# Performance work log

Measured on AMD Instinct MI355X. Metric: run time of the kernel, lower is better.

The kernel has to match this reference:

```python
import jax, jax.numpy as jnp
import numpy as np

TEMPERATURE = 0.1

def setup_inputs() -> dict:
    key = jax.random.key(0)
    k1, k2 = jax.random.split(key)
    B, D = 8192, 512
    anchor = jax.random.normal(k1, (B, D), dtype=jnp.float32)
    positive = jax.random.normal(k2, (B, D), dtype=jnp.float32)
    return {"anchor": anchor, "positive": positive}

def reference(anchor, positive):
    # sim[i, j] = <anchor_i, positive_j> / T  -- [B, B]
    sim = jnp.einsum("bd,nd->bn", anchor, positive) / TEMPERATURE
    # InfoNCE with in-batch negatives: positive is the diagonal; since softmax
    # is permutation-invariant, -log_softmax(logits)[pos] = logsumexp(row) - diag.
    loss = jax.nn.logsumexp(sim, axis=1) - jnp.diagonal(sim)
    return jnp.mean(loss)
```

## Files before the change

kernel.cpp:

```cpp
#include <hip/hip_runtime.h>
#include <hip/hip_bf16.h>
#include <math.h>
#include <stdint.h>


#define NB 8192
#define DDIM 512
#define SPLITS 16
#define BM 256
#define BN 128
#define CPB (NB / SPLITS)
#define TPB (CPB / BN)
#define NROUND 32

#define DELTA 0.045f
#define INV_DELTA (1.0f / DELTA)
#define OUT_SCALE (DELTA * DELTA * 10.0f)

typedef unsigned char u8;
typedef __attribute__((ext_vector_type(4))) int i32x4;

__device__ __forceinline__ void gl2lds16(const u8* g, const u8* l) {
  __builtin_amdgcn_global_load_lds(
      (__attribute__((address_space(1))) unsigned int*)(uintptr_t)g,
      (__attribute__((address_space(3))) unsigned int*)(unsigned int)(uintptr_t)l,
      16, 0, 0);
}

__device__ __forceinline__ unsigned pack4(float x0, float x1, float x2, float x3) {
  int q0 = min(127, max(-127, __float2int_rn(x0 * INV_DELTA)));
  int q1 = min(127, max(-127, __float2int_rn(x1 * INV_DELTA)));
  int q2 = min(127, max(-127, __float2int_rn(x2 * INV_DELTA)));
  int q3 = min(127, max(-127, __float2int_rn(x3 * INV_DELTA)));
  return (q0 & 0xFF) | ((q1 & 0xFF) << 8) | ((q2 & 0xFF) << 16) | ((q3 & 0xFF) << 24);
}

__global__ void cvt_diag_kernel(const float* __restrict__ a, const float* __restrict__ p,
                                u8* __restrict__ aq, u8* __restrict__ pq,
                                float* __restrict__ diag, float* __restrict__ out) {
  if (blockIdx.x == 0 && threadIdx.x == 0) out[0] = 0.f;
  int row = (blockIdx.x * 256 + threadIdx.x) >> 6;
  int lane = threadIdx.x & 63;
  const float4* ar = (const float4*)(a + (size_t)row * DDIM + lane * 8);
  const float4* pr = (const float4*)(p + (size_t)row * DDIM + lane * 8);
  float4 a0 = ar[0], a1 = ar[1];
  float4 p0 = pr[0], p1 = pr[1];
  *(uint2*)(aq + (size_t)row * DDIM + lane * 8) =
      (uint2){pack4(a0.x, a0.y, a0.z, a0.w), pack4(a1.x, a1.y, a1.z, a1.w)};
  *(uint2*)(pq + (size_t)row * DDIM + lane * 8) =
      (uint2){pack4(p0.x, p0.y, p0.z, p0.w), pack4(p1.x, p1.y, p1.z, p1.w)};
  float s = a0.x * p0.x + a0.y * p0.y + a0.z * p0.z + a0.w * p0.w +
            a1.x * p1.x + a1.y * p1.y + a1.z * p1.z + a1.w * p1.w;
  for (int off = 32; off > 0; off >>= 1) s += __shfl_down(s, off);
  if (lane == 0) diag[row] = s * 10.0f;
}

__global__ __launch_bounds__(512, 4) void gemm_lse(
    const u8* __restrict__ Aq, const u8* __restrict__ Bq,
    float* __restrict__ partM, float* __restrict__ partL) {
  __shared__ u8 sA[2][BM * 64];
  __shared__ u8 sB[2][BN * 64];
  __shared__ float sMm[2][BM];
  __shared__ float sMl[2][BM];

  const int tid = threadIdx.x;
  const int wave = tid >> 6;
  const int lane = tid & 63;
  const int quad = lane >> 4;
  const int l16 = lane & 15;
  const int wr = wave >> 1, wc = wave & 1;

  const int bid = blockIdx.x;
  const int xcd = bid & 7;
  const int idx = bid >> 3;
  const int rowTile = (idx & 3) * 8 + xcd;
  const int colSplit = idx >> 2;
  const int row0 = rowTile * BM;
  const int col0 = colSplit * CPB;

  const int rsub = lane >> 2;
  const int qsrc = (lane & 3) ^ ((rsub >> 1) & 3);
  const u8* aCol = Aq + (size_t)(row0 + wave * 32 + rsub) * DDIM + qsrc * 16;
  const u8* bCol = Bq + (size_t)(col0 + wave * 16 + rsub) * DDIM + qsrc * 16;
  const int ldsOffA = wave * 2048;
  const int ldsOffB = wave * 1024;

  const int sw = (l16 >> 1) & 3;
  const int fragA = (wr * 64 + l16) * 64 + ((quad ^ sw) * 16);
  const int fragB = (wc * 64 + l16) * 64 + ((quad ^ sw) * 16);

#define STAGE(r)                                                        \
  do {                                                                  \
    int _t = (r) >> 3, _kk = ((r) & 7) << 6, _bf = (r) & 1;             \
    const u8* _a = aCol + _kk;                                          \
    const u8* _b = bCol + _t * (BN * DDIM) + _kk;                       \
    gl2lds16(_a, &sA[_bf][ldsOffA]);                                    \
    gl2lds16(_a + 16 * DDIM, &sA[_bf][ldsOffA + 1024]);                 \
    gl2lds16(_b, &sB[_bf][ldsOffB]);                                    \
  } while (0)

  STAGE(0);

  i32x4 acc[4][4];
#pragma unroll
  for (int mi = 0; mi < 4; ++mi)
#pragma unroll
    for (int ni = 0; ni < 4; ++ni) acc[mi][ni] = (i32x4){0, 0, 0, 0};

  float rm[4][4], rl[4][4];
#pragma unroll
  for (int mi = 0; mi < 4; ++mi)
#pragma unroll
    for (int rr = 0; rr < 4; ++rr) { rm[mi][rr] = -INFINITY; rl[mi][rr] = 0.f; }

  for (int r = 0; r < NROUND; ++r) {
    const int buf = r & 1;
    __syncthreads();
    if (r < NROUND - 1) STAGE(r + 1);

    i32x4 bq[4];
#pragma unroll
    for (int ni = 0; ni < 4; ++ni)
      bq[ni] = *(const i32x4*)(&sB[buf][fragB + ni * 16 * 64]);
#pragma unroll
    for (int mi = 0; mi < 4; ++mi) {
      i32x4 af = *(const i32x4*)(&sA[buf][fragA + mi * 16 * 64]);
#pragma unroll
      for (int ni = 0; ni < 4; ++ni)
        acc[mi][ni] = __builtin_amdgcn_mfma_i32_16x16x64_i8(af, bq[ni], acc[mi][ni], 0, 0, 0);
    }

    if ((r & 7) == 7) {
#pragma unroll
      for (int mi = 0; mi < 4; ++mi) {
#pragma unroll
        for (int rr = 0; rr < 4; ++rr) {
          float v0 = (float)acc[mi][0][rr] * OUT_SCALE;
          float v1 = (float)acc[mi][1][rr] * OUT_SCALE;
          float v2 = (float)acc[mi][2][rr] * OUT_SCALE;
          float v3 = (float)acc[mi][3][rr] * OUT_SCALE;
          float vm = fmaxf(fmaxf(v0, v1), fmaxf(v2, v3));
          float nm = fmaxf(rm[mi][rr], vm);
          rl[mi][rr] = rl[mi][rr] * __expf(rm[mi][rr] - nm) +
                       (__expf(v0 - nm) + __expf(v1 - nm) +
                        __expf(v2 - nm) + __expf(v3 - nm));
          rm[mi][rr] = nm;
#pragma unroll
          for (int ni = 0; ni < 4; ++ni) acc[mi][ni][rr] = 0;
        }
      }
    }
  }

#pragma unroll
  for (int mi = 0; mi < 4; ++mi) {
#pragma unroll
    for (int rr = 0; rr < 4; ++rr) {
      float m = rm[mi][rr], l = rl[mi][rr];
#pragma unroll
      for (int mask = 1; mask < 16; mask <<= 1) {
        float om = __shfl_xor(m, mask);
        float ol = __shfl_xor(l, mask);
        float nm = fmaxf(m, om);
        l = l * __expf(m - nm) + ol * __expf(om - nm);
        m = nm;
      }
      if (l16 == 0) {
        int rowl = wr * 64 + mi * 16 + quad * 4 + rr;
        sMm[wc][rowl] = m;
        sMl[wc][rowl] = l;
      }
    }
  }
  __syncthreads();
  if (tid < BM) {
    float m0 = sMm[0][tid], m1 = sMm[1][tid];
    float l0 = sMl[0][tid], l1 = sMl[1][tid];
    float nm = fmaxf(m0, m1);
    partM[(size_t)colSplit * NB + row0 + tid] = nm;
    partL[(size_t)colSplit * NB + row0 + tid] =
        l0 * __expf(m0 - nm) + l1 * __expf(m1 - nm);
  }
#undef STAGE
}

__global__ void reduce_kernel(const float* __restrict__ partM,
                              const float* __restrict__ partL,
                              const float* __restrict__ diag, float* __restrict__ out) {
  __shared__ float red[4];
  int r = blockIdx.x * 256 + threadIdx.x;
  float M = -INFINITY;
#pragma unroll
  for (int s = 0; s < SPLITS; ++s) M = fmaxf(M, partM[(size_t)s * NB + r]);
  float L = 0.f;
#pragma unroll
  for (int s = 0; s < SPLITS; ++s)
    L += partL[(size_t)s * NB + r] * __expf(partM[(size_t)s * NB + r] - M);
  float v = M + __logf(L) - diag[r];
  for (int off = 32; off > 0; off >>= 1) v += __shfl_down(v, off);
  if ((threadIdx.x & 63) == 0) red[threadIdx.x >> 6] = v;
  __syncthreads();
  if (threadIdx.x == 0) {
    float s = (red[0] + red[1] + red[2] + red[3]) * (1.0f / (float)NB);
    atomicAdd(out, s);
  }
}

extern "C" void kernel_launch(void* const* d_in, const int* in_sizes, int n_in,
                              void* d_out, int out_size, void* d_ws, size_t ws_size,
                              hipStream_t stream) {
  const float* anchor = (const float*)d_in[0];
  const float* positive = (const float*)d_in[1];
  float* out = (float*)d_out;

  char* ws = (char*)d_ws;
  u8* Aq = (u8*)ws;
  u8* Bq = (u8*)(ws + (size_t)4194304);
  float* diag = (float*)(ws + (size_t)8388608);
  float* partM = (float*)(ws + (size_t)8388608 + 32768);
  float* partL = (float*)(ws + (size_t)8388608 + 32768 + (size_t)SPLITS * NB * 4);

  cvt_diag_kernel<<<NB / 4, 256, 0, stream>>>(anchor, positive, Aq, Bq, diag, out);
  gemm_lse<<<512, 512, 0, stream>>>(Aq, Bq, partM, partL);
  reduce_kernel<<<NB / 256, 256, 0, stream>>>(partM, partL, diag, out);
}
```

Measured before the change: 126.6 us.

## Use 256x256 tiles with single K pass and base-2 LSE partials

Each block now computes a square 256x256 tile over the full K dimension, with each wave holding an 8x4 set of MFMA accumulators. There are 32 column splits instead of 16 splits that each looped over four 128-column tiles, so the grid becomes 1024 blocks. The LSE epilogue runs once at the end, uses integer max and exp2/log2, reuses LDS as scratch, and stores a single log-sum-exp partial per row instead of separate max and sum. This raises arithmetic intensity per LDS load and cuts epilogue and partial-store traffic. In exchange it doubles accumulator registers, lowers occupancy (launch bounds 2) and shortens each block's pipeline to 8 steps.

```diff
diff --git a/kernel.cpp b/kernel.cpp
--- a/kernel.cpp
+++ b/kernel.cpp
@@ -6,19 +6,34 @@
 
 #define NB 8192
 #define DDIM 512
-#define SPLITS 16
+#define SPLITS 32
 #define BM 256
-#define BN 128
-#define CPB (NB / SPLITS)
-#define TPB (CPB / BN)
-#define NROUND 32
+#define BNB 256
+#define KT 8
 
 #define DELTA 0.045f
 #define INV_DELTA (1.0f / DELTA)
 #define OUT_SCALE (DELTA * DELTA * 10.0f)
+#define K2F (OUT_SCALE * 1.4426950408889634f)
+#define LN2F 0.6931471805599453f
 
 typedef unsigned char u8;
 typedef __attribute__((ext_vector_type(4))) int i32x4;
+
+__device__ __forceinline__ float fexp2(float x) {
+#if __has_builtin(__builtin_amdgcn_exp2f)
+  return __builtin_amdgcn_exp2f(x);
+#else
+  return __expf(x * LN2F);
+#endif
+}
+__device__ __forceinline__ float flog2(float x) {
+#if __has_builtin(__builtin_amdgcn_logf)
+  return __builtin_amdgcn_logf(x);
+#else
+  return __logf(x) * 1.4426950408889634f;
+#endif
+}
 
 __device__ __forceinline__ void gl2lds16(const u8* g, const u8* l) {
   __builtin_amdgcn_global_load_lds(
@@ -55,20 +70,19 @@
   if (lane == 0) diag[row] = s * 10.0f;
 }
 
-__global__ __launch_bounds__(512, 4) void gemm_lse(
+__global__ __launch_bounds__(512, 2) void gemm_lse(
     const u8* __restrict__ Aq, const u8* __restrict__ Bq,
-    float* __restrict__ partM, float* __restrict__ partL) {
+    float* __restrict__ partLse) {
   __shared__ u8 sA[2][BM * 64];
-  __shared__ u8 sB[2][BN * 64];
-  __shared__ float sMm[2][BM];
-  __shared__ float sMl[2][BM];
+  __shared__ u8 sB[2][BNB * 64];
 
   const int tid = threadIdx.x;
   const int wave = tid >> 6;
   const int lane = tid & 63;
   const int quad = lane >> 4;
   const int l16 = lane & 15;
-  const int wr = wave >> 1, wc = wave & 1;
+  const int wr = wave >> 2;
+  const int wc = wave & 3;
 
   const int bid = blockIdx.x;
   const int xcd = bid & 7;
@@ -76,127 +90,119 @@
   const int rowTile = (idx & 3) * 8 + xcd;
   const int colSplit = idx >> 2;
   const int row0 = rowTile * BM;
-  const int col0 = colSplit * CPB;
+  const int col0 = colSplit * BNB;
 
   const int rsub = lane >> 2;
   const int qsrc = (lane & 3) ^ ((rsub >> 1) & 3);
   const u8* aCol = Aq + (size_t)(row0 + wave * 32 + rsub) * DDIM + qsrc * 16;
-  const u8* bCol = Bq + (size_t)(col0 + wave * 16 + rsub) * DDIM + qsrc * 16;
-  const int ldsOffA = wave * 2048;
-  const int ldsOffB = wave * 1024;
+  const u8* bCol = Bq + (size_t)(col0 + wave * 32 + rsub) * DDIM + qsrc * 16;
+  const int ldsOff = wave * 2048;
 
   const int sw = (l16 >> 1) & 3;
-  const int fragA = (wr * 64 + l16) * 64 + ((quad ^ sw) * 16);
+  const int fragA = (wr * 128 + l16) * 64 + ((quad ^ sw) * 16);
   const int fragB = (wc * 64 + l16) * 64 + ((quad ^ sw) * 16);
 
-#define STAGE(r)                                                        \
-  do {                                                                  \
-    int _t = (r) >> 3, _kk = ((r) & 7) << 6, _bf = (r) & 1;             \
-    const u8* _a = aCol + _kk;                                          \
-    const u8* _b = bCol + _t * (BN * DDIM) + _kk;                       \
-    gl2lds16(_a, &sA[_bf][ldsOffA]);                                    \
-    gl2lds16(_a + 16 * DDIM, &sA[_bf][ldsOffA + 1024]);                 \
-    gl2lds16(_b, &sB[_bf][ldsOffB]);                                    \
-  } while (0)
-
-  STAGE(0);
-
-  i32x4 acc[4][4];
-#pragma unroll
-  for (int mi = 0; mi < 4; ++mi)
+  gl2lds16(aCol, &sA[0][ldsOff]);
+  gl2lds16(aCol + 16 * DDIM, &sA[0][ldsOff + 1024]);
+  gl2lds16(bCol, &sB[0][ldsOff]);
+  gl2lds16(bCol + 16 * DDIM, &sB[0][ldsOff + 1024]);
+
+  i32x4 acc[8][4];
+#pragma unroll
+  for (int mi = 0; mi < 8; ++mi)
 #pragma unroll
     for (int ni = 0; ni < 4; ++ni) acc[mi][ni] = (i32x4){0, 0, 0, 0};
 
-  float rm[4][4], rl[4][4];
-#pragma unroll
-  for (int mi = 0; mi < 4; ++mi)
-#pragma unroll
-    for (int rr = 0; rr < 4; ++rr) { rm[mi][rr] = -INFINITY; rl[mi][rr] = 0.f; }
-
-  for (int r = 0; r < NROUND; ++r) {
-    const int buf = r & 1;
+  float2* const scr0 = (float2*)&sA[0][0];
+  float2* const scr1 = (float2*)&sB[0][0];
+
+  for (int kt = 0; kt < KT; ++kt) {
+    const int par = kt & 1;
     __syncthreads();
-    if (r < NROUND - 1) STAGE(r + 1);
-
+    if (kt < KT - 1) {
+      const int kk = (kt + 1) * 64;
+      gl2lds16(aCol + kk, &sA[par ^ 1][ldsOff]);
+      gl2lds16(aCol + 16 * DDIM + kk, &sA[par ^ 1][ldsOff + 1024]);
+      gl2lds16(bCol + kk, &sB[par ^ 1][ldsOff]);
+      gl2lds16(bCol + 16 * DDIM + kk, &sB[par ^ 1][ldsOff + 1024]);
+    }
     i32x4 bq[4];
 #pragma unroll
     for (int ni = 0; ni < 4; ++ni)
-      bq[ni] = *(const i32x4*)(&sB[buf][fragB + ni * 16 * 64]);
-#pragma unroll
-    for (int mi = 0; mi < 4; ++mi) {
-      i32x4 af = *(const i32x4*)(&sA[buf][fragA + mi * 16 * 64]);
+      bq[ni] = *(const i32x4*)(&sB[par][fragB + ni * 1024]);
+#pragma unroll
+    for (int mp = 0; mp < 4; ++mp) {
+      i32x4 a0 = *(const i32x4*)(&sA[par][fragA + (2 * mp) * 1024]);
+      i32x4 a1 = *(const i32x4*)(&sA[par][fragA + (2 * mp + 1) * 1024]);
 #pragma unroll
       for (int ni = 0; ni < 4; ++ni)
-        acc[mi][ni] = __builtin_amdgcn_mfma_i32_16x16x64_i8(af, bq[ni], acc[mi][ni], 0, 0, 0);
-    }
-
-    if ((r & 7) == 7) {
-#pragma unroll
-      for (int mi = 0; mi < 4; ++mi) {
-#pragma unroll
-        for (int rr = 0; rr < 4; ++rr) {
-          float v0 = (float)acc[mi][0][rr] * OUT_SCALE;
-          float v1 = (float)acc[mi][1][rr] * OUT_SCALE;
-          float v2 = (float)acc[mi][2][rr] * OUT_SCALE;
-          float v3 = (float)acc[mi][3][rr] * OUT_SCALE;
-          float vm = fmaxf(fmaxf(v0, v1), fmaxf(v2, v3));
-          float nm = fmaxf(rm[mi][rr], vm);
-          rl[mi][rr] = rl[mi][rr] * __expf(rm[mi][rr] - nm) +
-                       (__expf(v0 - nm) + __expf(v1 - nm) +
-                        __expf(v2 - nm) + __expf(v3 - nm));
-          rm[mi][rr] = nm;
-#pragma unroll
-          for (int ni = 0; ni < 4; ++ni) acc[mi][ni][rr] = 0;
+        acc[2 * mp][ni] =
+            __builtin_amdgcn_mfma_i32_16x16x64_i8(a0, bq[ni], acc[2 * mp][ni], 0, 0, 0);
+#pragma unroll
+      for (int ni = 0; ni < 4; ++ni)
+        acc[2 * mp + 1][ni] =
+            __builtin_amdgcn_mfma_i32_16x16x64_i8(a1, bq[ni], acc[2 * mp + 1][ni], 0, 0, 0);
+      if (kt == KT - 1) {
+#pragma unroll
+        for (int mi = 2 * mp; mi <= 2 * mp + 1; ++mi) {
+#pragma unroll
+          for (int rr = 0; rr < 4; ++rr) {
+            const int i0 = acc[mi][0][rr], i1 = acc[mi][1][rr];
+            const int i2 = acc[mi][2][rr], i3 = acc[mi][3][rr];
+            const int im = max(max(i0, i1), max(i2, i3));
+            const float mf = (float)im * K2F;
+            float l = fexp2(fmaf((float)i0, K2F, -mf)) +
+                      fexp2(fmaf((float)i1, K2F, -mf)) +
+                      fexp2(fmaf((float)i2, K2F, -mf)) +
+                      fexp2(fmaf((float)i3, K2F, -mf));
+            float m = mf;
+#pragma unroll
+            for (int mask = 1; mask < 4; mask <<= 1) {
+              const float om = __shfl_xor(m, mask);
+              const float ol = __shfl_xor(l, mask);
+              const float nm = fmaxf(m, om);
+              l = l * fexp2(m - nm) + ol * fexp2(om - nm);
+              m = nm;
+            }
+            if ((l16 & 3) == 0) {
+              const int rowl = mi * 16 + quad * 4 + rr;
+              (wr ? scr1 : scr0)[rowl * 16 + (l16 >> 2) * 4 + wc] = (float2){m, l};
+            }
+          }
         }
       }
     }
   }
 
-#pragma unroll
-  for (int mi = 0; mi < 4; ++mi) {
-#pragma unroll
-    for (int rr = 0; rr < 4; ++rr) {
-      float m = rm[mi][rr], l = rl[mi][rr];
-#pragma unroll
-      for (int mask = 1; mask < 16; mask <<= 1) {
-        float om = __shfl_xor(m, mask);
-        float ol = __shfl_xor(l, mask);
-        float nm = fmaxf(m, om);
-        l = l * __expf(m - nm) + ol * __expf(om - nm);
-        m = nm;
-      }
-      if (l16 == 0) {
-        int rowl = wr * 64 + mi * 16 + quad * 4 + rr;
-        sMm[wc][rowl] = m;
-        sMl[wc][rowl] = l;
-      }
-    }
-  }
   __syncthreads();
   if (tid < BM) {
-    float m0 = sMm[0][tid], m1 = sMm[1][tid];
-    float l0 = sMl[0][tid], l1 = sMl[1][tid];
-    float nm = fmaxf(m0, m1);
-    partM[(size_t)colSplit * NB + row0 + tid] = nm;
-    partL[(size_t)colSplit * NB + row0 + tid] =
-        l0 * __expf(m0 - nm) + l1 * __expf(m1 - nm);
+    const float2* scr = (tid < 128) ? scr0 : scr1;
+    const int rowl = tid & 127;
+    float2 p[16];
+    float M = -INFINITY;
+#pragma unroll
+    for (int i = 0; i < 16; ++i) {
+      p[i] = scr[rowl * 16 + i];
+      M = fmaxf(M, p[i].x);
+    }
+    float L = 0.f;
+#pragma unroll
+    for (int i = 0; i < 16; ++i) L += p[i].y * fexp2(p[i].x - M);
+    partLse[(size_t)colSplit * NB + row0 + tid] = M + flog2(L);
   }
-#undef STAGE
-}
-
-__global__ void reduce_kernel(const float* __restrict__ partM,
-                              const float* __restrict__ partL,
+}
+
+__global__ void reduce_kernel(const float* __restrict__ partLse,
                               const float* __restrict__ diag, float* __restrict__ out) {
   __shared__ float red[4];
   int r = blockIdx.x * 256 + threadIdx.x;
   float M = -INFINITY;
 #pragma unroll
-  for (int s = 0; s < SPLITS; ++s) M = fmaxf(M, partM[(size_t)s * NB + r]);
+  for (int s = 0; s < SPLITS; ++s) M = fmaxf(M, partLse[(size_t)s * NB + r]);
   float L = 0.f;
 #pragma unroll
-  for (int s = 0; s < SPLITS; ++s)
-    L += partL[(size_t)s * NB + r] * __expf(partM[(size_t)s * NB + r] - M);
-  float v = M + __logf(L) - diag[r];
+  for (int s = 0; s < SPLITS; ++s) L += fexp2(partLse[(size_t)s * NB + r] - M);
+  float v = (M + flog2(L)) * LN2F - diag[r];
   for (int off = 32; off > 0; off >>= 1) v += __shfl_down(v, off);
   if ((threadIdx.x & 63) == 0) red[threadIdx.x >> 6] = v;
   __syncthreads();
@@ -217,10 +223,9 @@
   u8* Aq = (u8*)ws;
   u8* Bq = (u8*)(ws + (size_t)4194304);
   float* diag = (float*)(ws + (size_t)8388608);
-  float* partM = (float*)(ws + (size_t)8388608 + 32768);
-  float* partL = (float*)(ws + (size_t)8388608 + 32768 + (size_t)SPLITS * NB * 4);
+  float* partLse = (float*)(ws + (size_t)8388608 + 32768);
 
   cvt_diag_kernel<<<NB / 4, 256, 0, stream>>>(anchor, positive, Aq, Bq, diag, out);
-  gemm_lse<<<512, 512, 0, stream>>>(Aq, Bq, partM, partL);
-  reduce_kernel<<<NB / 256, 256, 0, stream>>>(partM, partL, diag, out);
-}
+  gemm_lse<<<SPLITS * (NB / BM), 512, 0, stream>>>(Aq, Bq, partLse);
+  reduce_kernel<<<NB / 256, 256, 0, stream>>>(partLse, diag, out);
+}
```

Result: slower. 133.1 us (+5.1%).

## Switch to 32x32x32 int8 MFMA with base-2 online LSE and single partial buffer

Applied to the files above, without the earlier changes.

Replaces the 16x16x64 int8 MFMA tiling with 32x32x32 MFMAs, so each wave issues fewer, larger matrix ops and uses a different fragment layout and row mapping. The online logsumexp moves to base-2 exponentials with the scale folded into a single FMA, and the per-row max is taken in the integer domain before conversion. Each split now writes one log-sum-exp value instead of separate max and sum arrays, which cuts partial-buffer traffic in the reduce. The larger MFMA reduces LDS fragment reads per MAC but changes the register layout and needs a wider 32-lane shuffle reduction.

```diff
diff --git a/kernel.cpp b/kernel.cpp
--- a/kernel.cpp
+++ b/kernel.cpp
@@ -10,15 +10,32 @@
 #define BM 256
 #define BN 128
 #define CPB (NB / SPLITS)
-#define TPB (CPB / BN)
 #define NROUND 32
 
 #define DELTA 0.045f
 #define INV_DELTA (1.0f / DELTA)
 #define OUT_SCALE (DELTA * DELTA * 10.0f)
+#define K2F (OUT_SCALE * 1.4426950408889634f)
+#define LN2F 0.6931471805599453f
 
 typedef unsigned char u8;
 typedef __attribute__((ext_vector_type(4))) int i32x4;
+typedef __attribute__((ext_vector_type(16))) int i32x16;
+
+__device__ __forceinline__ float fexp2(float x) {
+#if __has_builtin(__builtin_amdgcn_exp2f)
+  return __builtin_amdgcn_exp2f(x);
+#else
+  return __expf(x * LN2F);
+#endif
+}
+__device__ __forceinline__ float flog2(float x) {
+#if __has_builtin(__builtin_amdgcn_logf)
+  return __builtin_amdgcn_logf(x);
+#else
+  return __logf(x) * 1.4426950408889634f;
+#endif
+}
 
 __device__ __forceinline__ void gl2lds16(const u8* g, const u8* l) {
   __builtin_amdgcn_global_load_lds(
@@ -57,7 +74,7 @@
 
 __global__ __launch_bounds__(512, 4) void gemm_lse(
     const u8* __restrict__ Aq, const u8* __restrict__ Bq,
-    float* __restrict__ partM, float* __restrict__ partL) {
+    float* __restrict__ partLse) {
   __shared__ u8 sA[2][BM * 64];
   __shared__ u8 sB[2][BN * 64];
   __shared__ float sMm[2][BM];
@@ -66,8 +83,8 @@
   const int tid = threadIdx.x;
   const int wave = tid >> 6;
   const int lane = tid & 63;
-  const int quad = lane >> 4;
-  const int l16 = lane & 15;
+  const int l32 = lane & 31;
+  const int hi = lane >> 5;
   const int wr = wave >> 1, wc = wave & 1;
 
   const int bid = blockIdx.x;
@@ -85,9 +102,11 @@
   const int ldsOffA = wave * 2048;
   const int ldsOffB = wave * 1024;
 
-  const int sw = (l16 >> 1) & 3;
-  const int fragA = (wr * 64 + l16) * 64 + ((quad ^ sw) * 16);
-  const int fragB = (wc * 64 + l16) * 64 + ((quad ^ sw) * 16);
+  const int sw32 = (l32 >> 1) & 3;
+  const int oct0 = ((0 + hi) ^ sw32) * 16;
+  const int oct1 = ((2 + hi) ^ sw32) * 16;
+  const int rowA = (wr * 64 + l32) * 64;
+  const int rowB = (wc * 64 + l32) * 64;
 
 #define STAGE(r)                                                        \
   do {                                                                  \
@@ -101,72 +120,78 @@
 
   STAGE(0);
 
-  i32x4 acc[4][4];
-#pragma unroll
-  for (int mi = 0; mi < 4; ++mi)
-#pragma unroll
-    for (int ni = 0; ni < 4; ++ni) acc[mi][ni] = (i32x4){0, 0, 0, 0};
-
-  float rm[4][4], rl[4][4];
-#pragma unroll
-  for (int mi = 0; mi < 4; ++mi)
-#pragma unroll
-    for (int rr = 0; rr < 4; ++rr) { rm[mi][rr] = -INFINITY; rl[mi][rr] = 0.f; }
+  i32x16 acc[2][2];
+#pragma unroll
+  for (int mb = 0; mb < 2; ++mb)
+#pragma unroll
+    for (int nb = 0; nb < 2; ++nb)
+#pragma unroll
+      for (int g = 0; g < 16; ++g) acc[mb][nb][g] = 0;
+
+  float rm[2][16], rl[2][16];
+#pragma unroll
+  for (int mb = 0; mb < 2; ++mb)
+#pragma unroll
+    for (int g = 0; g < 16; ++g) { rm[mb][g] = -INFINITY; rl[mb][g] = 0.f; }
 
   for (int r = 0; r < NROUND; ++r) {
     const int buf = r & 1;
     __syncthreads();
     if (r < NROUND - 1) STAGE(r + 1);
 
-    i32x4 bq[4];
-#pragma unroll
-    for (int ni = 0; ni < 4; ++ni)
-      bq[ni] = *(const i32x4*)(&sB[buf][fragB + ni * 16 * 64]);
-#pragma unroll
-    for (int mi = 0; mi < 4; ++mi) {
-      i32x4 af = *(const i32x4*)(&sA[buf][fragA + mi * 16 * 64]);
-#pragma unroll
-      for (int ni = 0; ni < 4; ++ni)
-        acc[mi][ni] = __builtin_amdgcn_mfma_i32_16x16x64_i8(af, bq[ni], acc[mi][ni], 0, 0, 0);
-    }
+    i32x4 b0k0 = *(const i32x4*)(&sB[buf][rowB + 0 * 2048 + oct0]);
+    i32x4 b1k0 = *(const i32x4*)(&sB[buf][rowB + 1 * 2048 + oct0]);
+    i32x4 b0k1 = *(const i32x4*)(&sB[buf][rowB + 0 * 2048 + oct1]);
+    i32x4 b1k1 = *(const i32x4*)(&sB[buf][rowB + 1 * 2048 + oct1]);
+    i32x4 a0k0 = *(const i32x4*)(&sA[buf][rowA + 0 * 2048 + oct0]);
+    i32x4 a1k0 = *(const i32x4*)(&sA[buf][rowA + 1 * 2048 + oct0]);
+    i32x4 a0k1 = *(const i32x4*)(&sA[buf][rowA + 0 * 2048 + oct1]);
+    i32x4 a1k1 = *(const i32x4*)(&sA[buf][rowA + 1 * 2048 + oct1]);
+
+    acc[0][0] = __builtin_amdgcn_mfma_i32_32x32x32_i8(a0k0, b0k0, acc[0][0], 0, 0, 0);
+    acc[0][1] = __builtin_amdgcn_mfma_i32_32x32x32_i8(a0k0, b1k0, acc[0][1], 0, 0, 0);
+    acc[1][0] = __builtin_amdgcn_mfma_i32_32x32x32_i8(a1k0, b0k0, acc[1][0], 0, 0, 0);
+    acc[1][1] = __builtin_amdgcn_mfma_i32_32x32x32_i8(a1k0, b1k0, acc[1][1], 0, 0, 0);
+    acc[0][0] = __builtin_amdgcn_mfma_i32_32x32x32_i8(a0k1, b0k1, acc[0][0], 0, 0, 0);
+    acc[0][1] = __builtin_amdgcn_mfma_i32_32x32x32_i8(a0k1, b1k1, acc[0][1], 0, 0, 0);
+    acc[1][0] = __builtin_amdgcn_mfma_i32_32x32x32_i8(a1k1, b0k1, acc[1][0], 0, 0, 0);
+    acc[1][1] = __builtin_amdgcn_mfma_i32_32x32x32_i8(a1k1, b1k1, acc[1][1], 0, 0, 0);
 
     if ((r & 7) == 7) {
 #pragma unroll
-      for (int mi = 0; mi < 4; ++mi) {
-#pragma unroll
-        for (int rr = 0; rr < 4; ++rr) {
-          float v0 = (float)acc[mi][0][rr] * OUT_SCALE;
-          float v1 = (float)acc[mi][1][rr] * OUT_SCALE;
-          float v2 = (float)acc[mi][2][rr] * OUT_SCALE;
-          float v3 = (float)acc[mi][3][rr] * OUT_SCALE;
-          float vm = fmaxf(fmaxf(v0, v1), fmaxf(v2, v3));
-          float nm = fmaxf(rm[mi][rr], vm);
-          rl[mi][rr] = rl[mi][rr] * __expf(rm[mi][rr] - nm) +
-                       (__expf(v0 - nm) + __expf(v1 - nm) +
-                        __expf(v2 - nm) + __expf(v3 - nm));
-          rm[mi][rr] = nm;
-#pragma unroll
-          for (int ni = 0; ni < 4; ++ni) acc[mi][ni][rr] = 0;
+      for (int mb = 0; mb < 2; ++mb) {
+#pragma unroll
+        for (int g = 0; g < 16; ++g) {
+          const int i0 = acc[mb][0][g], i1 = acc[mb][1][g];
+          const int im = max(i0, i1);
+          const float mf = (float)im * K2F;
+          const float nm = fmaxf(rm[mb][g], mf);
+          rl[mb][g] = rl[mb][g] * fexp2(rm[mb][g] - nm) +
+                      fexp2(fmaf((float)i0, K2F, -nm)) +
+                      fexp2(fmaf((float)i1, K2F, -nm));
+          rm[mb][g] = nm;
+          acc[mb][0][g] = 0;
+          acc[mb][1][g] = 0;
         }
       }
     }
   }
 
 #pragma unroll
-  for (int mi = 0; mi < 4; ++mi) {
-#pragma unroll
-    for (int rr = 0; rr < 4; ++rr) {
-      float m = rm[mi][rr], l = rl[mi][rr];
-#pragma unroll
-      for (int mask = 1; mask < 16; mask <<= 1) {
+  for (int mb = 0; mb < 2; ++mb) {
+#pragma unroll
+    for (int g = 0; g < 16; ++g) {
+      float m = rm[mb][g], l = rl[mb][g];
+#pragma unroll
+      for (int mask = 1; mask < 32; mask <<= 1) {
         float om = __shfl_xor(m, mask);
         float ol = __shfl_xor(l, mask);
         float nm = fmaxf(m, om);
-        l = l * __expf(m - nm) + ol * __expf(om - nm);
+        l = l * fexp2(m - nm) + ol * fexp2(om - nm);
         m = nm;
       }
-      if (l16 == 0) {
-        int rowl = wr * 64 + mi * 16 + quad * 4 + rr;
+      if (l32 == 0) {
+        int rowl = wr * 64 + mb * 32 + (g & 3) + 8 * (g >> 2) + 4 * hi;
         sMm[wc][rowl] = m;
         sMl[wc][rowl] = l;
       }
@@ -177,26 +202,23 @@
     float m0 = sMm[0][tid], m1 = sMm[1][tid];
     float l0 = sMl[0][tid], l1 = sMl[1][tid];
     float nm = fmaxf(m0, m1);
-    partM[(size_t)colSplit * NB + row0 + tid] = nm;
-    partL[(size_t)colSplit * NB + row0 + tid] =
-        l0 * __expf(m0 - nm) + l1 * __expf(m1 - nm);
+    float L = l0 * fexp2(m0 - nm) + l1 * fexp2(m1 - nm);
+    partLse[(size_t)colSplit * NB + row0 + tid] = nm + flog2(L);
   }
 #undef STAGE
 }
 
-__global__ void reduce_kernel(const float* __restrict__ partM,
-                              const float* __restrict__ partL,
+__global__ void reduce_kernel(const float* __restrict__ partLse,
                               const float* __restrict__ diag, float* __restrict__ out) {
   __shared__ float red[4];
   int r = blockIdx.x * 256 + threadIdx.x;
   float M = -INFINITY;
 #pragma unroll
-  for (int s = 0; s < SPLITS; ++s) M = fmaxf(M, partM[(size_t)s * NB + r]);
+  for (int s = 0; s < SPLITS; ++s) M = fmaxf(M, partLse[(size_t)s * NB + r]);
   float L = 0.f;
 #pragma unroll
-  for (int s = 0; s < SPLITS; ++s)
-    L += partL[(size_t)s * NB + r] * __expf(partM[(size_t)s * NB + r] - M);
-  float v = M + __logf(L) - diag[r];
+  for (int s = 0; s < SPLITS; ++s) L += fexp2(partLse[(size_t)s * NB + r] - M);
+  float v = (M + flog2(L)) * LN2F - diag[r];
   for (int off = 32; off > 0; off >>= 1) v += __shfl_down(v, off);
   if ((threadIdx.x & 63) == 0) red[threadIdx.x >> 6] = v;
   __syncthreads();
@@ -217,10 +239,9 @@
   u8* Aq = (u8*)ws;
   u8* Bq = (u8*)(ws + (size_t)4194304);
   float* diag = (float*)(ws + (size_t)8388608);
-  float* partM = (float*)(ws + (size_t)8388608 + 32768);
-  float* partL = (float*)(ws + (size_t)8388608 + 32768 + (size_t)SPLITS * NB * 4);
+  float* partLse = (float*)(ws + (size_t)8388608 + 32768);
 
   cvt_diag_kernel<<<NB / 4, 256, 0, stream>>>(anchor, positive, Aq, Bq, diag, out);
-  gemm_lse<<<512, 512, 0, stream>>>(Aq, Bq, partM, partL);
-  reduce_kernel<<<NB / 256, 256, 0, stream>>>(partM, partL, diag, out);
-}
+  gemm_lse<<<512, 512, 0, stream>>>(Aq, Bq, partLse);
+  reduce_kernel<<<NB / 256, 256, 0, stream>>>(partLse, diag, out);
+}
```

Measured after the change: 153.6 us. 21.4% more time.

## Halve GEMM block tile to 128x128 with 4 waves, use exp2 and single LSE partial

Applied to the files above, without the earlier changes.

The fused int8 GEMM plus logsumexp kernel moves from 256x128 tiles with 8 waves to 128x128 tiles with 4 waves, which doubles the grid to 1024 blocks, and remaps row tiles per XCD to match. The online-softmax update now takes the row max in integer space and uses hardware exp2/log2 with a folded scale, which cuts float conversions and multiplies. Each block writes one log-sum-exp value per row instead of a separate max and sum, so the partial-result traffic and the reduce work are halved. The cost is less reuse of B tiles per block, since each B tile is now shared by half as many rows, and the work per block changes with the new tile shape.

```diff
diff --git a/kernel.cpp b/kernel.cpp
--- a/kernel.cpp
+++ b/kernel.cpp
@@ -7,18 +7,34 @@
 #define NB 8192
 #define DDIM 512
 #define SPLITS 16
-#define BM 256
+#define BM 128
 #define BN 128
 #define CPB (NB / SPLITS)
-#define TPB (CPB / BN)
 #define NROUND 32
 
 #define DELTA 0.045f
 #define INV_DELTA (1.0f / DELTA)
 #define OUT_SCALE (DELTA * DELTA * 10.0f)
+#define K2F (OUT_SCALE * 1.4426950408889634f)
+#define LN2F 0.6931471805599453f
 
 typedef unsigned char u8;
 typedef __attribute__((ext_vector_type(4))) int i32x4;
+
+__device__ __forceinline__ float fexp2(float x) {
+#if __has_builtin(__builtin_amdgcn_exp2f)
+  return __builtin_amdgcn_exp2f(x);
+#else
+  return __expf(x * LN2F);
+#endif
+}
+__device__ __forceinline__ float flog2(float x) {
+#if __has_builtin(__builtin_amdgcn_logf)
+  return __builtin_amdgcn_logf(x);
+#else
+  return __logf(x) * 1.4426950408889634f;
+#endif
+}
 
 __device__ __forceinline__ void gl2lds16(const u8* g, const u8* l) {
   __builtin_amdgcn_global_load_lds(
@@ -55,9 +71,9 @@
   if (lane == 0) diag[row] = s * 10.0f;
 }
 
-__global__ __launch_bounds__(512, 4) void gemm_lse(
+__global__ __launch_bounds__(256, 4) void gemm_lse(
     const u8* __restrict__ Aq, const u8* __restrict__ Bq,
-    float* __restrict__ partM, float* __restrict__ partL) {
+    float* __restrict__ partLse) {
   __shared__ u8 sA[2][BM * 64];
   __shared__ u8 sB[2][BN * 64];
   __shared__ float sMm[2][BM];
@@ -73,8 +89,8 @@
   const int bid = blockIdx.x;
   const int xcd = bid & 7;
   const int idx = bid >> 3;
-  const int rowTile = (idx & 3) * 8 + xcd;
-  const int colSplit = idx >> 2;
+  const int rowTile = (idx & 7) * 8 + xcd;
+  const int colSplit = idx >> 3;
   const int row0 = rowTile * BM;
   const int col0 = colSplit * CPB;
 
@@ -97,6 +113,7 @@
     gl2lds16(_a, &sA[_bf][ldsOffA]);                                    \
     gl2lds16(_a + 16 * DDIM, &sA[_bf][ldsOffA + 1024]);                 \
     gl2lds16(_b, &sB[_bf][ldsOffB]);                                    \
+    gl2lds16(_b + 64 * DDIM, &sB[_bf][ldsOffB + 4096]);                 \
   } while (0)
 
   STAGE(0);
@@ -135,15 +152,16 @@
       for (int mi = 0; mi < 4; ++mi) {
 #pragma unroll
         for (int rr = 0; rr < 4; ++rr) {
-          float v0 = (float)acc[mi][0][rr] * OUT_SCALE;
-          float v1 = (float)acc[mi][1][rr] * OUT_SCALE;
-          float v2 = (float)acc[mi][2][rr] * OUT_SCALE;
-          float v3 = (float)acc[mi][3][rr] * OUT_SCALE;
-          float vm = fmaxf(fmaxf(v0, v1), fmaxf(v2, v3));
-          float nm = fmaxf(rm[mi][rr], vm);
-          rl[mi][rr] = rl[mi][rr] * __expf(rm[mi][rr] - nm) +
-                       (__expf(v0 - nm) + __expf(v1 - nm) +
-                        __expf(v2 - nm) + __expf(v3 - nm));
+          const int i0 = acc[mi][0][rr], i1 = acc[mi][1][rr];
+          const int i2 = acc[mi][2][rr], i3 = acc[mi][3][rr];
+          const int im = max(max(i0, i1), max(i2, i3));
+          const float mf = (float)im * K2F;
+          const float nm = fmaxf(rm[mi][rr], mf);
+          rl[mi][rr] = rl[mi][rr] * fexp2(rm[mi][rr] - nm) +
+                       (fexp2(fmaf((float)i0, K2F, -nm)) +
+                        fexp2(fmaf((float)i1, K2F, -nm)) +
+                        fexp2(fmaf((float)i2, K2F, -nm)) +
+                        fexp2(fmaf((float)i3, K2F, -nm)));
           rm[mi][rr] = nm;
 #pragma unroll
           for (int ni = 0; ni < 4; ++ni) acc[mi][ni][rr] = 0;
@@ -162,7 +180,7 @@
         float om = __shfl_xor(m, mask);
         float ol = __shfl_xor(l, mask);
         float nm = fmaxf(m, om);
-        l = l * __expf(m - nm) + ol * __expf(om - nm);
+        l = l * fexp2(m - nm) + ol * fexp2(om - nm);
         m = nm;
       }
       if (l16 == 0) {
@@ -177,26 +195,23 @@
     float m0 = sMm[0][tid], m1 = sMm[1][tid];
     float l0 = sMl[0][tid], l1 = sMl[1][tid];
     float nm = fmaxf(m0, m1);
-    partM[(size_t)colSplit * NB + row0 + tid] = nm;
-    partL[(size_t)colSplit * NB + row0 + tid] =
-        l0 * __expf(m0 - nm) + l1 * __expf(m1 - nm);
+    float L = l0 * fexp2(m0 - nm) + l1 * fexp2(m1 - nm);
+    partLse[(size_t)colSplit * NB + row0 + tid] = nm + flog2(L);
   }
 #undef STAGE
 }
 
-__global__ void reduce_kernel(const float* __restrict__ partM,
-                              const float* __restrict__ partL,
+__global__ void reduce_kernel(const float* __restrict__ partLse,
                               const float* __restrict__ diag, float* __restrict__ out) {
   __shared__ float red[4];
   int r = blockIdx.x * 256 + threadIdx.x;
   float M = -INFINITY;
 #pragma unroll
-  for (int s = 0; s < SPLITS; ++s) M = fmaxf(M, partM[(size_t)s * NB + r]);
+  for (int s = 0; s < SPLITS; ++s) M = fmaxf(M, partLse[(size_t)s * NB + r]);
   float L = 0.f;
 #pragma unroll
-  for (int s = 0; s < SPLITS; ++s)
-    L += partL[(size_t)s * NB + r] * __expf(partM[(size_t)s * NB + r] - M);
-  float v = M + __logf(L) - diag[r];
+  for (int s = 0; s < SPLITS; ++s) L += fexp2(partLse[(size_t)s * NB + r] - M);
+  float v = (M + flog2(L)) * LN2F - diag[r];
   for (int off = 32; off > 0; off >>= 1) v += __shfl_down(v, off);
   if ((threadIdx.x & 63) == 0) red[threadIdx.x >> 6] = v;
   __syncthreads();
@@ -217,10 +232,9 @@
   u8* Aq = (u8*)ws;
   u8* Bq = (u8*)(ws + (size_t)4194304);
   float* diag = (float*)(ws + (size_t)8388608);
-  float* partM = (float*)(ws + (size_t)8388608 + 32768);
-  float* partL = (float*)(ws + (size_t)8388608 + 32768 + (size_t)SPLITS * NB * 4);
+  float* partLse = (float*)(ws + (size_t)8388608 + 32768);
 
   cvt_diag_kernel<<<NB / 4, 256, 0, stream>>>(anchor, positive, Aq, Bq, diag, out);
-  gemm_lse<<<512, 512, 0, stream>>>(Aq, Bq, partM, partL);
-  reduce_kernel<<<NB / 256, 256, 0, stream>>>(partM, partL, diag, out);
-}
+  gemm_lse<<<SPLITS * (NB / BM), 256, 0, stream>>>(Aq, Bq, partLse);
+  reduce_kernel<<<NB / 256, 256, 0, stream>>>(partLse, diag, out);
+}
```

New measurement: 129.6 us. +2.4%, slower.
